# Optimization experiments

Hardware: AMD Instinct MI355X
Metric: run time of the kernel (lower is better)

## Reference

```python
import jax, jax.numpy as jnp
import numpy as np

N_NODES = 50000
N_FEAT = 128
HIDDEN = 3
N_EDGES = 600000
N_POWERS = 3


def setup_inputs() -> dict:
    key = jax.random.key(0)
    ks = jax.random.split(key, 6)
    x = jax.random.normal(ks[0], (N_NODES, N_FEAT), dtype=jnp.float32)
    edge_index = jax.random.randint(ks[1], (N_POWERS, 2, N_EDGES), 0, N_NODES, dtype=jnp.int64)
    # MLP params for the 3 adjacency powers, stacked on the leading axis.
    # torch Linear(in,out) stored transposed here: y = x @ W + b.
    Wa = jax.random.normal(ks[2], (N_POWERS, N_FEAT, HIDDEN), dtype=jnp.float32) * (1.0 / np.sqrt(N_FEAT))
    ba = jax.random.normal(ks[3], (N_POWERS, HIDDEN), dtype=jnp.float32) * 0.01
    Wb = jax.random.normal(ks[4], (N_POWERS, HIDDEN, 1), dtype=jnp.float32) * (1.0 / np.sqrt(HIDDEN))
    bb = jax.random.normal(ks[5], (N_POWERS, 1), dtype=jnp.float32) * 0.01
    return {"x": x, "edge_index": edge_index, "Wa": Wa, "ba": ba, "Wb": Wb, "bb": bb}


def reference(x, edge_index, Wa, ba, Wb, bb):
    # Gather source/target node features per edge, per adjacency power.
    x_j = x[edge_index[:, 0]]          # [P, E, F]
    x_i = x[edge_index[:, 1]]          # [P, E, F]
    abs_dif = jnp.abs(x_j - x_i)       # [P, E, F]
    # Tiny per-edge MLP: Linear -> ReLU -> Linear -> Sigmoid (separate params per power).
    h = jax.nn.relu(jnp.einsum('pef,pfh->peh', abs_dif, Wa) + ba[:, None, :])  # [P, E, H]
    w = jax.nn.sigmoid(jnp.einsum('peh,pho->peo', h, Wb) + bb[:, None, :])     # [P, E, 1]
    return w[..., 0]                   # [P, E] edge weights for each power
```

## Files before the change

kernel.cpp:

```cpp
#include <hip/hip_runtime.h>
#include <math.h>

#define N_NODES 50000
#define N_FEAT  128
#define N_EDGES 600000
#define N_POWERS 3

#define PAIRS 5
#define EDGES_PER_BLK (64 * PAIRS)

#define CAP 81920
#define NBUCK 8
#define CHUNK 2048
#define NCHUNK 293

typedef _Float16 half2v __attribute__((ext_vector_type(2)));
union HU { unsigned u; half2v h; };

__device__ __forceinline__ int bucket_of(int j) { return (int)(((unsigned)j * 41u) >> 18); }

__global__ __launch_bounds__(256) void conv_x_plain(const float* __restrict__ x,
                                                    unsigned* __restrict__ xh,
                                                    const float* __restrict__ Wa,
                                                    unsigned* __restrict__ wah) {
    const int t = blockIdx.x * 256 + threadIdx.x;
    const float4* x4 = (const float4*)x;
    float4 a = x4[(size_t)t * 2];
    float4 b = x4[(size_t)t * 2 + 1];
    HU p0, p1, p2, p3;
    p0.h = half2v{(_Float16)a.x, (_Float16)a.y};
    p1.h = half2v{(_Float16)a.z, (_Float16)a.w};
    p2.h = half2v{(_Float16)b.x, (_Float16)b.y};
    p3.h = half2v{(_Float16)b.z, (_Float16)b.w};
    ((uint4*)xh)[t] = uint4{p0.u, p1.u, p2.u, p3.u};
    if (blockIdx.x == 0 && threadIdx.x < 192) {
        const int tt = threadIdx.x;
        #pragma unroll
        for (int q = 0; q < 3; ++q) {
            int idx = tt + q * 192;
            int c  = idx % 3;
            int pk = idx / 3;
            int k  = pk % 64;
            int p  = pk / 64;
            float w0 = Wa[p * 384 + (2 * k) * 3 + c];
            float w1 = Wa[p * 384 + (2 * k + 1) * 3 + c];
            HU u; u.h = half2v{(_Float16)w0, (_Float16)w1};
            wah[idx] = u.u;
        }
    }
}

__global__ __launch_bounds__(256) void hist_kernel(const int* __restrict__ edge_index,
                                                   int* __restrict__ hist) {
    __shared__ int lh[NBUCK];
    const int p = blockIdx.y, chunk = blockIdx.x;
    if (threadIdx.x < NBUCK) lh[threadIdx.x] = 0;
    __syncthreads();
    const int* ej = edge_index + (size_t)p * 2 * N_EDGES;
    const int base = chunk * CHUNK;
    #pragma unroll
    for (int k = 0; k < 8; ++k) {
        const int e = base + k * 256 + threadIdx.x;
        if (e < N_EDGES) {
            const int j = __builtin_nontemporal_load(ej + e);
            atomicAdd(&lh[bucket_of(j)], 1);
        }
    }
    __syncthreads();
    if (threadIdx.x < NBUCK)
        hist[(p * NBUCK + threadIdx.x) * NCHUNK + chunk] = lh[threadIdx.x];
}

__global__ __launch_bounds__(64) void scan_hist(int* __restrict__ hist,
                                                int* __restrict__ cur) {
    const int pb = blockIdx.x;
    const int lane = threadIdx.x;
    int* h = hist + pb * NCHUNK;
    int carry = 0;
    for (int t = 0; t < NCHUNK; t += 64) {
        const int c = t + lane;
        int v = (c < NCHUNK) ? h[c] : 0;
        int s = v;
        #pragma unroll
        for (int d = 1; d < 64; d <<= 1) {
            int u = __shfl_up(s, d, 64);
            if (lane >= d) s += u;
        }
        if (c < NCHUNK) h[c] = carry + (s - v);
        carry += __shfl(s, 63, 64);
    }
    if (lane == 0) cur[pb] = carry;
}

__global__ __launch_bounds__(256) void scatter_pass(const int* __restrict__ edge_index,
                                                    const int* __restrict__ hist,
                                                    unsigned long long* __restrict__ su) {
    __shared__ int lc[NBUCK];
    const int p = blockIdx.y, chunk = blockIdx.x;
    if (threadIdx.x < NBUCK) lc[threadIdx.x] = 0;
    __syncthreads();
    const int* ej = edge_index + (size_t)p * 2 * N_EDGES;
    const int* ei = ej + N_EDGES;
    const int base = chunk * CHUNK;
    #pragma unroll
    for (int k = 0; k < 8; ++k) {
        const int e = base + k * 256 + threadIdx.x;
        if (e < N_EDGES) {
            const int j = __builtin_nontemporal_load(ej + e);
            const int i = __builtin_nontemporal_load(ei + e);
            const int b = bucket_of(j);
            const int pos = atomicAdd(&lc[b], 1);
            const int off = hist[(p * NBUCK + b) * NCHUNK + chunk];
            const size_t slot = (size_t)(p * NBUCK + b) * CAP + off + pos;
            su[slot] = (unsigned long long)(unsigned)(j | (i << 16))
                     | ((unsigned long long)e << 32);
        }
    }
}

template<int PAT>
__device__ __forceinline__ float swz(float v) {
    return __int_as_float(__builtin_amdgcn_ds_swizzle(__float_as_int(v), PAT));
}

__device__ __forceinline__ void dot3_8(const uint4& qa0, const uint4& qa1,
                                       const uint4& qb0, const uint4& qb1,
                                       const HU wa[8][3],
                                       float& h0, float& h1, float& h2) {
    unsigned ua[8] = {qa0.x, qa0.y, qa0.z, qa0.w, qa1.x, qa1.y, qa1.z, qa1.w};
    unsigned ub[8] = {qb0.x, qb0.y, qb0.z, qb0.w, qb1.x, qb1.y, qb1.z, qb1.w};
    h0 = 0.f; h1 = 0.f; h2 = 0.f;
    #pragma unroll
    for (int k = 0; k < 8; ++k) {
        HU a, b, d;
        a.u = ua[k]; b.u = ub[k];
        d.h = a.h - b.h;
        d.u &= 0x7fff7fffu;
        h0 = __builtin_amdgcn_fdot2(d.h, wa[k][0].h, h0, false);
        h1 = __builtin_amdgcn_fdot2(d.h, wa[k][1].h, h1, false);
        h2 = __builtin_amdgcn_fdot2(d.h, wa[k][2].h, h2, false);
    }
}

__global__ __launch_bounds__(256) void adj_kernel_sorted(
    const unsigned* __restrict__ xh,
    const unsigned long long* __restrict__ su,
    const int* __restrict__ cur,
    const unsigned* __restrict__ wah,
    const float* __restrict__ ba,
    const float* __restrict__ Wb,
    const float* __restrict__ bb,
    float* __restrict__ out)
{
    const int p    = blockIdx.y;
    const int b    = blockIdx.x & 7;
    const int k    = blockIdx.x >> 3;
    const int tid  = threadIdx.x;
    const int lane = tid & 63;
    const int wave = tid >> 6;
    const int sub  = lane & 7;
    const int grp  = lane >> 3;

    const int count = cur[p * NBUCK + b];
    const int base  = k * EDGES_PER_BLK;
    if (base >= count) return;

    HU wa[8][3];
    {
        const unsigned* wp = wah + ((size_t)p * 64 + sub * 8) * 3;
        #pragma unroll
        for (int kk = 0; kk < 8; ++kk) {
            wa[kk][0].u = wp[kk * 3 + 0];
            wa[kk][1].u = wp[kk * 3 + 1];
            wa[kk][2].u = wp[kk * 3 + 2];
        }
        #pragma unroll
        for (int kk = 0; kk < 8; ++kk) {
            asm volatile("" : "+v"(wa[kk][0].u), "+v"(wa[kk][1].u), "+v"(wa[kk][2].u));
        }
    }

    const float ba0 = ba[p * 3 + 0], ba1 = ba[p * 3 + 1], ba2 = ba[p * 3 + 2];
    const float wb0 = Wb[p * 3 + 0], wb1 = Wb[p * 3 + 1], wb2 = Wb[p * 3 + 2];
    const float bbp = bb[p];

    const unsigned long long* sup = su + (size_t)(p * NBUCK + b) * CAP;
    float* outp = out + (size_t)p * N_EDGES;

    const int eoff = wave * 8 + grp;
    const int roff = sub * 8;
    const int cm1  = count - 1;

    #pragma unroll
    for (int it = 0; it < PAIRS; ++it) {
        const int r1 = base + it * 64 + eoff;
        const int r2 = r1 + 32;
        const bool v1 = r1 < count;
        const bool v2 = r2 < count;
        const int s1 = min(r1, cm1);
        const int s2 = min(r2, cm1);

        const unsigned long long q1 = __builtin_nontemporal_load(sup + s1);
        const unsigned long long q2 = __builtin_nontemporal_load(sup + s2);
        const int j1 = (int)(q1 & 0xFFFFu);
        const int i1 = (int)((q1 >> 16) & 0xFFFFu);
        const int e1 = (int)(q1 >> 32);
        const int j2 = (int)(q2 & 0xFFFFu);
        const int i2 = (int)((q2 >> 16) & 0xFFFFu);
        const int e2 = (int)(q2 >> 32);

        const uint4* rj1 = (const uint4*)(xh + ((size_t)j1 << 6) + roff);
        const uint4* ri1 = (const uint4*)(xh + ((size_t)i1 << 6) + roff);
        const uint4* rj2 = (const uint4*)(xh + ((size_t)j2 << 6) + roff);
        const uint4* ri2 = (const uint4*)(xh + ((size_t)i2 << 6) + roff);
        uint4 a0 = rj1[0], a1 = rj1[1];
        uint4 b0 = ri1[0], b1 = ri1[1];
        uint4 c0 = rj2[0], c1 = rj2[1];
        uint4 d0 = ri2[0], d1 = ri2[1];

        float h0a, h1a, h2a, h0b, h1b, h2b;
        dot3_8(a0, a1, b0, b1, wa, h0a, h1a, h2a);
        dot3_8(c0, c1, d0, d1, wa, h0b, h1b, h2b);

        h0a += swz<0x041F>(h0a); h1a += swz<0x041F>(h1a); h2a += swz<0x041F>(h2a);
        h0b += swz<0x041F>(h0b); h1b += swz<0x041F>(h1b); h2b += swz<0x041F>(h2b);
        h0a += swz<0x081F>(h0a); h1a += swz<0x081F>(h1a); h2a += swz<0x081F>(h2a);
        h0b += swz<0x081F>(h0b); h1b += swz<0x081F>(h1b); h2b += swz<0x081F>(h2b);
        h0a += swz<0x101F>(h0a); h1a += swz<0x101F>(h1a); h2a += swz<0x101F>(h2a);
        h0b += swz<0x101F>(h0b); h1b += swz<0x101F>(h1b); h2b += swz<0x101F>(h2b);

        if (sub == 0) {
            if (v1) {
                float r0 = fmaxf(h0a + ba0, 0.f);
                float r1f = fmaxf(h1a + ba1, 0.f);
                float r2f = fmaxf(h2a + ba2, 0.f);
                float s  = fmaf(r0, wb0, fmaf(r1f, wb1, fmaf(r2f, wb2, bbp)));
                __builtin_nontemporal_store(1.f / (1.f + __expf(-s)), outp + e1);
            }
            if (v2) {
                float r0 = fmaxf(h0b + ba0, 0.f);
                float r1f = fmaxf(h1b + ba1, 0.f);
                float r2f = fmaxf(h2b + ba2, 0.f);
                float s  = fmaf(r0, wb0, fmaf(r1f, wb1, fmaf(r2f, wb2, bbp)));
                __builtin_nontemporal_store(1.f / (1.f + __expf(-s)), outp + e2);
            }
        }
    }
}

__global__ __launch_bounds__(256) void adj_kernel_f16(
    const unsigned* __restrict__ xh,
    const unsigned* __restrict__ wah,
    const int*   __restrict__ edge_index,
    const float* __restrict__ ba,
    const float* __restrict__ Wb,
    const float* __restrict__ bb,
    float* __restrict__ out)
{
    const int p    = blockIdx.y;
    const int tid  = threadIdx.x;
    const int lane = tid & 63;
    const int wave = tid >> 6;
    const int sub  = lane & 7;
    const int grp  = lane >> 3;

    HU wa[8][3];
    {
        const unsigned* wp = wah + ((size_t)p * 64 + sub * 8) * 3;
        #pragma unroll
        for (int k = 0; k < 8; ++k) {
            wa[k][0].u = wp[k * 3 + 0];
            wa[k][1].u = wp[k * 3 + 1];
            wa[k][2].u = wp[k * 3 + 2];
        }
        #pragma unroll
        for (int k = 0; k < 8; ++k) {
            asm volatile("" : "+v"(wa[k][0].u), "+v"(wa[k][1].u), "+v"(wa[k][2].u));
        }
    }

    const float ba0 = ba[p * 3 + 0], ba1 = ba[p * 3 + 1], ba2 = ba[p * 3 + 2];
    const float wb0 = Wb[p * 3 + 0], wb1 = Wb[p * 3 + 1], wb2 = Wb[p * 3 + 2];
    const float bbp = bb[p];

    const int* ej = edge_index + (size_t)p * 2 * N_EDGES;
    const int* ei = ej + N_EDGES;
    float* outp = out + (size_t)p * N_EDGES;

    const int e_blk = blockIdx.x * EDGES_PER_BLK;
    const int eoff  = wave * 8 + grp;
    const int roff  = sub * 8;

    #pragma unroll
    for (int it = 0; it < PAIRS; ++it) {
        const int e1 = e_blk + it * 64 + eoff;
        const int e2 = e1 + 32;
        const int j1 = __builtin_nontemporal_load(ej + e1);
        const int i1 = __builtin_nontemporal_load(ei + e1);
        const int j2 = __builtin_nontemporal_load(ej + e2);
        const int i2 = __builtin_nontemporal_load(ei + e2);

        const uint4* rj1 = (const uint4*)(xh + ((size_t)j1 << 6) + roff);
        const uint4* ri1 = (const uint4*)(xh + ((size_t)i1 << 6) + roff);
        const uint4* rj2 = (const uint4*)(xh + ((size_t)j2 << 6) + roff);
        const uint4* ri2 = (const uint4*)(xh + ((size_t)i2 << 6) + roff);
        uint4 a0 = rj1[0], a1 = rj1[1];
        uint4 b0 = ri1[0], b1 = ri1[1];
        uint4 c0 = rj2[0], c1 = rj2[1];
        uint4 d0 = ri2[0], d1 = ri2[1];

        float h0a, h1a, h2a, h0b, h1b, h2b;
        dot3_8(a0, a1, b0, b1, wa, h0a, h1a, h2a);
        dot3_8(c0, c1, d0, d1, wa, h0b, h1b, h2b);

        h0a += swz<0x041F>(h0a); h1a += swz<0x041F>(h1a); h2a += swz<0x041F>(h2a);
        h0b += swz<0x041F>(h0b); h1b += swz<0x041F>(h1b); h2b += swz<0x041F>(h2b);
        h0a += swz<0x081F>(h0a); h1a += swz<0x081F>(h1a); h2a += swz<0x081F>(h2a);
        h0b += swz<0x081F>(h0b); h1b += swz<0x081F>(h1b); h2b += swz<0x081F>(h2b);
        h0a += swz<0x101F>(h0a); h1a += swz<0x101F>(h1a); h2a += swz<0x101F>(h2a);
        h0b += swz<0x101F>(h0b); h1b += swz<0x101F>(h1b); h2b += swz<0x101F>(h2b);

        if (sub == 0) {
            float r0 = fmaxf(h0a + ba0, 0.f);
            float r1 = fmaxf(h1a + ba1, 0.f);
            float r2 = fmaxf(h2a + ba2, 0.f);
            float s  = fmaf(r0, wb0, fmaf(r1, wb1, fmaf(r2, wb2, bbp)));
            __builtin_nontemporal_store(1.f / (1.f + __expf(-s)), outp + e1);
            r0 = fmaxf(h0b + ba0, 0.f);
            r1 = fmaxf(h1b + ba1, 0.f);
            r2 = fmaxf(h2b + ba2, 0.f);
            s  = fmaf(r0, wb0, fmaf(r1, wb1, fmaf(r2, wb2, bbp)));
            __builtin_nontemporal_store(1.f / (1.f + __expf(-s)), outp + e2);
        }
    }
}

__global__ __launch_bounds__(256) void adj_kernel_f32(
    const float* __restrict__ x,
    const int*   __restrict__ edge_index,
    const float* __restrict__ Wa,
    const float* __restrict__ ba,
    const float* __restrict__ Wb,
    const float* __restrict__ bb,
    float* __restrict__ out)
{
    const int p    = blockIdx.y;
    const int tid  = threadIdx.x;
    const int lane = tid & 63;
    const int wave = tid >> 6;
    const int sub  = lane & 15;
    const int grp  = lane >> 4;
    const int f0 = sub * 8;

    const float* Wap = Wa + (size_t)p * N_FEAT * 3;
    float wa0[8], wa1[8], wa2[8];
    #pragma unroll
    for (int k = 0; k < 8; ++k) {
        wa0[k] = Wap[(f0 + k) * 3 + 0];
        wa1[k] = Wap[(f0 + k) * 3 + 1];
        wa2[k] = Wap[(f0 + k) * 3 + 2];
    }
    const float ba0 = ba[p * 3 + 0], ba1 = ba[p * 3 + 1], ba2 = ba[p * 3 + 2];
    const float wb0 = Wb[p * 3 + 0], wb1 = Wb[p * 3 + 1], wb2 = Wb[p * 3 + 2];
    const float bbp = bb[p];

    const int e = blockIdx.x * 16 + wave * 4 + grp;
    const int* ej = edge_index + (size_t)p * 2 * N_EDGES;
    const int* ei = ej + N_EDGES;
    const int j = ej[e];
    const int i = ei[e];

    const float4* xj = (const float4*)(x + (size_t)j * N_FEAT + f0);
    const float4* xi = (const float4*)(x + (size_t)i * N_FEAT + f0);
    float4 a0 = xj[0], a1 = xj[1];
    float4 b0 = xi[0], b1 = xi[1];

    float d[8];
    d[0] = fabsf(a0.x - b0.x); d[1] = fabsf(a0.y - b0.y);
    d[2] = fabsf(a0.z - b0.z); d[3] = fabsf(a0.w - b0.w);
    d[4] = fabsf(a1.x - b1.x); d[5] = fabsf(a1.y - b1.y);
    d[6] = fabsf(a1.z - b1.z); d[7] = fabsf(a1.w - b1.w);

    float h0 = 0.f, h1 = 0.f, h2 = 0.f;
    #pragma unroll
    for (int k = 0; k < 8; ++k) {
        h0 = fmaf(d[k], wa0[k], h0);
        h1 = fmaf(d[k], wa1[k], h1);
        h2 = fmaf(d[k], wa2[k], h2);
    }
    #pragma unroll
    for (int m = 1; m < 16; m <<= 1) {
        h0 += __shfl_xor(h0, m, 64);
        h1 += __shfl_xor(h1, m, 64);
        h2 += __shfl_xor(h2, m, 64);
    }
    if (sub == 0) {
        float r0 = fmaxf(h0 + ba0, 0.f);
        float r1 = fmaxf(h1 + ba1, 0.f);
        float r2 = fmaxf(h2 + ba2, 0.f);
        float s  = fmaf(r0, wb0, fmaf(r1, wb1, fmaf(r2, wb2, bbp)));
        float w  = 1.f / (1.f + expf(-s));
        out[(size_t)p * N_EDGES + e] = w;
    }
}

extern "C" void kernel_launch(void* const* d_in, const int* in_sizes, int n_in,
                              void* d_out, int out_size, void* d_ws, size_t ws_size,
                              hipStream_t stream) {
    const float* x          = (const float*)d_in[0];
    const int*   edge_index = (const int*)d_in[1];
    const float* Wa         = (const float*)d_in[2];
    const float* ba         = (const float*)d_in[3];
    const float* Wb         = (const float*)d_in[4];
    const float* bb         = (const float*)d_in[5];
    float* out = (float*)d_out;

    const size_t x_bytes    = (size_t)N_NODES * N_FEAT * 2;
    const size_t su_bytes   = (size_t)N_POWERS * NBUCK * CAP * 8;
    const size_t wa_bytes   = 2304;
    const size_t hist_bytes = (size_t)N_POWERS * NBUCK * NCHUNK * 4;
    const size_t cur_bytes  = NBUCK * N_POWERS * 4;
    const size_t need_full  = x_bytes + su_bytes + wa_bytes + hist_bytes + cur_bytes;

    if (ws_size >= need_full) {
        char* w = (char*)d_ws;
        unsigned* xh = (unsigned*)w;
        unsigned long long* su = (unsigned long long*)(w + x_bytes);
        unsigned* wah = (unsigned*)(w + x_bytes + su_bytes);
        int* hist = (int*)(w + x_bytes + su_bytes + wa_bytes);
        int* cur  = (int*)(w + x_bytes + su_bytes + wa_bytes + hist_bytes);

        conv_x_plain<<<N_NODES * N_FEAT / 2048, 256, 0, stream>>>(x, xh, Wa, wah);
        hist_kernel<<<dim3(NCHUNK, N_POWERS), 256, 0, stream>>>(edge_index, hist);
        scan_hist<<<NBUCK * N_POWERS, 64, 0, stream>>>(hist, cur);
        scatter_pass<<<dim3(NCHUNK, N_POWERS), 256, 0, stream>>>(edge_index, hist, su);
        dim3 grid(NBUCK * (CAP / EDGES_PER_BLK), N_POWERS);
        adj_kernel_sorted<<<grid, 256, 0, stream>>>(xh, su, cur, wah, ba, Wb, bb, out);
    } else if (ws_size >= x_bytes + wa_bytes) {
        unsigned* xh  = (unsigned*)d_ws;
        unsigned* wah = (unsigned*)((char*)d_ws + x_bytes);
        conv_x_plain<<<N_NODES * N_FEAT / 2048, 256, 0, stream>>>(x, xh, Wa, wah);
        dim3 grid(N_EDGES / EDGES_PER_BLK, N_POWERS);
        adj_kernel_f16<<<grid, 256, 0, stream>>>(xh, wah, edge_index, ba, Wb, bb, out);
    } else {
        dim3 grid((N_EDGES + 15) / 16, N_POWERS);
        adj_kernel_f32<<<grid, 256, 0, stream>>>(x, edge_index, Wa, ba, Wb, bb, out);
    }
}
```

Measured before the change: 177.3 us.

## Aggregate bucket atomics per wave and software-pipeline gathers in sorted adjacency kernel

The histogram and scatter passes now group lanes by bucket using ballots. One leader per bucket does a single LDS atomic for the whole group, and scatter computes each lane's rank with popcount. The scatter pass also seeds its local counters with the chunk offsets, so it no longer reads hist per edge. The sorted adjacency kernel preloads all packed edge records up front and prefetches the next iteration's node feature rows while computing the current one, under a launch-bounds occupancy hint. This aims to cut LDS atomic contention and hide gather latency, at the cost of extra registers.

```diff
diff --git a/kernel.cpp b/kernel.cpp
--- a/kernel.cpp
+++ b/kernel.cpp
@@ -18,6 +18,17 @@
 union HU { unsigned u; half2v h; };
 
 __device__ __forceinline__ int bucket_of(int j) { return (int)(((unsigned)j * 41u) >> 18); }
+
+__device__ __forceinline__ unsigned long long match8(int b, bool valid) {
+    const unsigned long long m0 = __ballot(b & 1);
+    const unsigned long long m1 = __ballot(b & 2);
+    const unsigned long long m2 = __ballot(b & 4);
+    const unsigned long long vm = __ballot(valid);
+    unsigned long long m = (b & 1) ? m0 : ~m0;
+    m &= (b & 2) ? m1 : ~m1;
+    m &= (b & 4) ? m2 : ~m2;
+    return m & vm;
+}
 
 __global__ __launch_bounds__(256) void conv_x_plain(const float* __restrict__ x,
                                                     unsigned* __restrict__ xh,
@@ -58,13 +69,16 @@
     __syncthreads();
     const int* ej = edge_index + (size_t)p * 2 * N_EDGES;
     const int base = chunk * CHUNK;
+    const int lane = threadIdx.x & 63;
     #pragma unroll
     for (int k = 0; k < 8; ++k) {
         const int e = base + k * 256 + threadIdx.x;
-        if (e < N_EDGES) {
-            const int j = __builtin_nontemporal_load(ej + e);
-            atomicAdd(&lh[bucket_of(j)], 1);
-        }
+        const bool valid = e < N_EDGES;
+        const int j = __builtin_nontemporal_load(ej + (valid ? e : 0));
+        const int b = bucket_of(j);
+        const unsigned long long m = match8(b, valid);
+        if (valid && lane == (int)__builtin_ctzll(m))
+            atomicAdd(&lh[b], (int)__popcll(m));
     }
     __syncthreads();
     if (threadIdx.x < NBUCK)
@@ -97,21 +111,29 @@
                                                     unsigned long long* __restrict__ su) {
     __shared__ int lc[NBUCK];
     const int p = blockIdx.y, chunk = blockIdx.x;
-    if (threadIdx.x < NBUCK) lc[threadIdx.x] = 0;
+    if (threadIdx.x < NBUCK)
+        lc[threadIdx.x] = hist[(p * NBUCK + threadIdx.x) * NCHUNK + chunk];
     __syncthreads();
     const int* ej = edge_index + (size_t)p * 2 * N_EDGES;
     const int* ei = ej + N_EDGES;
     const int base = chunk * CHUNK;
+    const int lane = threadIdx.x & 63;
     #pragma unroll
     for (int k = 0; k < 8; ++k) {
         const int e = base + k * 256 + threadIdx.x;
-        if (e < N_EDGES) {
-            const int j = __builtin_nontemporal_load(ej + e);
-            const int i = __builtin_nontemporal_load(ei + e);
-            const int b = bucket_of(j);
-            const int pos = atomicAdd(&lc[b], 1);
-            const int off = hist[(p * NBUCK + b) * NCHUNK + chunk];
-            const size_t slot = (size_t)(p * NBUCK + b) * CAP + off + pos;
+        const bool valid = e < N_EDGES;
+        const int j = __builtin_nontemporal_load(ej + (valid ? e : 0));
+        const int i = __builtin_nontemporal_load(ei + (valid ? e : 0));
+        const int b = bucket_of(j);
+        const unsigned long long m = match8(b, valid);
+        const int ldr = m ? (int)__builtin_ctzll(m) : 0;
+        int basepos = 0;
+        if (valid && lane == ldr)
+            basepos = atomicAdd(&lc[b], (int)__popcll(m));
+        basepos = __shfl(basepos, ldr, 64);
+        if (valid) {
+            const int rank = (int)__popcll(m & ((1ull << lane) - 1ull));
+            const size_t slot = (size_t)(p * NBUCK + b) * CAP + basepos + rank;
             su[slot] = (unsigned long long)(unsigned)(j | (i << 16))
                      | ((unsigned long long)e << 32);
         }
@@ -142,7 +164,7 @@
     }
 }
 
-__global__ __launch_bounds__(256) void adj_kernel_sorted(
+__global__ __launch_bounds__(256, 4) void adj_kernel_sorted(
     const unsigned* __restrict__ xh,
     const unsigned long long* __restrict__ su,
     const int* __restrict__ cur,
@@ -191,36 +213,43 @@
     const int roff = sub * 8;
     const int cm1  = count - 1;
 
+    unsigned long long q[2 * PAIRS];
     #pragma unroll
     for (int it = 0; it < PAIRS; ++it) {
         const int r1 = base + it * 64 + eoff;
-        const int r2 = r1 + 32;
-        const bool v1 = r1 < count;
-        const bool v2 = r2 < count;
-        const int s1 = min(r1, cm1);
-        const int s2 = min(r2, cm1);
-
-        const unsigned long long q1 = __builtin_nontemporal_load(sup + s1);
-        const unsigned long long q2 = __builtin_nontemporal_load(sup + s2);
-        const int j1 = (int)(q1 & 0xFFFFu);
-        const int i1 = (int)((q1 >> 16) & 0xFFFFu);
-        const int e1 = (int)(q1 >> 32);
-        const int j2 = (int)(q2 & 0xFFFFu);
-        const int i2 = (int)((q2 >> 16) & 0xFFFFu);
-        const int e2 = (int)(q2 >> 32);
-
+        q[2 * it]     = __builtin_nontemporal_load(sup + min(r1, cm1));
+        q[2 * it + 1] = __builtin_nontemporal_load(sup + min(r1 + 32, cm1));
+    }
+
+    uint4 A0, A1, B0, B1, C0, C1, D0, D1;
+    {
+        const int j1 = (int)(q[0] & 0xFFFFu), i1 = (int)((q[0] >> 16) & 0xFFFFu);
+        const int j2 = (int)(q[1] & 0xFFFFu), i2 = (int)((q[1] >> 16) & 0xFFFFu);
         const uint4* rj1 = (const uint4*)(xh + ((size_t)j1 << 6) + roff);
         const uint4* ri1 = (const uint4*)(xh + ((size_t)i1 << 6) + roff);
         const uint4* rj2 = (const uint4*)(xh + ((size_t)j2 << 6) + roff);
         const uint4* ri2 = (const uint4*)(xh + ((size_t)i2 << 6) + roff);
-        uint4 a0 = rj1[0], a1 = rj1[1];
-        uint4 b0 = ri1[0], b1 = ri1[1];
-        uint4 c0 = rj2[0], c1 = rj2[1];
-        uint4 d0 = ri2[0], d1 = ri2[1];
+        A0 = rj1[0]; A1 = rj1[1]; B0 = ri1[0]; B1 = ri1[1];
+        C0 = rj2[0]; C1 = rj2[1]; D0 = ri2[0]; D1 = ri2[1];
+    }
+
+    #pragma unroll
+    for (int it = 0; it < PAIRS; ++it) {
+        uint4 nA0, nA1, nB0, nB1, nC0, nC1, nD0, nD1;
+        if (it + 1 < PAIRS) {
+            const int j1 = (int)(q[2 * it + 2] & 0xFFFFu), i1 = (int)((q[2 * it + 2] >> 16) & 0xFFFFu);
+            const int j2 = (int)(q[2 * it + 3] & 0xFFFFu), i2 = (int)((q[2 * it + 3] >> 16) & 0xFFFFu);
+            const uint4* rj1 = (const uint4*)(xh + ((size_t)j1 << 6) + roff);
+            const uint4* ri1 = (const uint4*)(xh + ((size_t)i1 << 6) + roff);
+            const uint4* rj2 = (const uint4*)(xh + ((size_t)j2 << 6) + roff);
+            const uint4* ri2 = (const uint4*)(xh + ((size_t)i2 << 6) + roff);
+            nA0 = rj1[0]; nA1 = rj1[1]; nB0 = ri1[0]; nB1 = ri1[1];
+            nC0 = rj2[0]; nC1 = rj2[1]; nD0 = ri2[0]; nD1 = ri2[1];
+        }
 
         float h0a, h1a, h2a, h0b, h1b, h2b;
-        dot3_8(a0, a1, b0, b1, wa, h0a, h1a, h2a);
-        dot3_8(c0, c1, d0, d1, wa, h0b, h1b, h2b);
+        dot3_8(A0, A1, B0, B1, wa, h0a, h1a, h2a);
+        dot3_8(C0, C1, D0, D1, wa, h0b, h1b, h2b);
 
         h0a += swz<0x041F>(h0a); h1a += swz<0x041F>(h1a); h2a += swz<0x041F>(h2a);
         h0b += swz<0x041F>(h0b); h1b += swz<0x041F>(h1b); h2b += swz<0x041F>(h2b);
@@ -230,20 +259,29 @@
         h0b += swz<0x101F>(h0b); h1b += swz<0x101F>(h1b); h2b += swz<0x101F>(h2b);
 
         if (sub == 0) {
-            if (v1) {
-                float r0 = fmaxf(h0a + ba0, 0.f);
+            const int r1 = base + it * 64 + eoff;
+            const int r2 = r1 + 32;
+            if (r1 < count) {
+                const int e1 = (int)(q[2 * it] >> 32);
+                float r0  = fmaxf(h0a + ba0, 0.f);
                 float r1f = fmaxf(h1a + ba1, 0.f);
                 float r2f = fmaxf(h2a + ba2, 0.f);
-                float s  = fmaf(r0, wb0, fmaf(r1f, wb1, fmaf(r2f, wb2, bbp)));
+                float s   = fmaf(r0, wb0, fmaf(r1f, wb1, fmaf(r2f, wb2, bbp)));
                 __builtin_nontemporal_store(1.f / (1.f + __expf(-s)), outp + e1);
             }
-            if (v2) {
-                float r0 = fmaxf(h0b + ba0, 0.f);
+            if (r2 < count) {
+                const int e2 = (int)(q[2 * it + 1] >> 32);
+                float r0  = fmaxf(h0b + ba0, 0.f);
                 float r1f = fmaxf(h1b + ba1, 0.f);
                 float r2f = fmaxf(h2b + ba2, 0.f);
-                float s  = fmaf(r0, wb0, fmaf(r1f, wb1, fmaf(r2f, wb2, bbp)));
+                float s   = fmaf(r0, wb0, fmaf(r1f, wb1, fmaf(r2f, wb2, bbp)));
                 __builtin_nontemporal_store(1.f / (1.f + __expf(-s)), outp + e2);
             }
+        }
+
+        if (it + 1 < PAIRS) {
+            A0 = nA0; A1 = nA1; B0 = nB0; B1 = nB1;
+            C0 = nC0; C1 = nC1; D0 = nD0; D1 = nD1;
         }
     }
 }
```

Result: no change. 175.0 us (-1.3%).

## Replace bucket sort with full counting sort by source node and unscatter outputs

Applied to the files above, without the earlier changes.

Swaps the 8-bucket partial sort for a full counting sort of edges by source node: per-node atomic counts, a 50k-element block scan, and an atomic scatter that also records each edge's inverse slot. The main kernel then walks edges in fully sorted order so the source-row gathers reuse cache, and it software-pipelines the next pair of row loads. Results are written in sorted order over the key buffer and permuted back by a new unscatter kernel. The cost is two extra launches, global atomics on node counters, a single-block-per-power serial scan, and a random-read gather pass for the outputs.

```diff
diff --git a/kernel.cpp b/kernel.cpp
--- a/kernel.cpp
+++ b/kernel.cpp
@@ -9,20 +9,15 @@
 #define PAIRS 5
 #define EDGES_PER_BLK (64 * PAIRS)
 
-#define CAP 81920
-#define NBUCK 8
-#define CHUNK 2048
-#define NCHUNK 293
-
 typedef _Float16 half2v __attribute__((ext_vector_type(2)));
+typedef unsigned u32x4  __attribute__((ext_vector_type(4)));
 union HU { unsigned u; half2v h; };
-
-__device__ __forceinline__ int bucket_of(int j) { return (int)(((unsigned)j * 41u) >> 18); }
 
 __global__ __launch_bounds__(256) void conv_x_plain(const float* __restrict__ x,
                                                     unsigned* __restrict__ xh,
                                                     const float* __restrict__ Wa,
-                                                    unsigned* __restrict__ wah) {
+                                                    unsigned* __restrict__ wah,
+                                                    int* __restrict__ cnt) {
     const int t = blockIdx.x * 256 + threadIdx.x;
     const float4* x4 = (const float4*)x;
     float4 a = x4[(size_t)t * 2];
@@ -33,6 +28,8 @@
     p2.h = half2v{(_Float16)b.x, (_Float16)b.y};
     p3.h = half2v{(_Float16)b.z, (_Float16)b.w};
     ((uint4*)xh)[t] = uint4{p0.u, p1.u, p2.u, p3.u};
+    if (cnt != nullptr && t < N_POWERS * N_NODES)
+        cnt[t] = 0;
     if (blockIdx.x == 0 && threadIdx.x < 192) {
         const int tt = threadIdx.x;
         #pragma unroll
@@ -50,72 +47,62 @@
     }
 }
 
-__global__ __launch_bounds__(256) void hist_kernel(const int* __restrict__ edge_index,
-                                                   int* __restrict__ hist) {
-    __shared__ int lh[NBUCK];
-    const int p = blockIdx.y, chunk = blockIdx.x;
-    if (threadIdx.x < NBUCK) lh[threadIdx.x] = 0;
+__global__ __launch_bounds__(1024) void count_kernel(const int* __restrict__ edge_index,
+                                                     int* __restrict__ cnt) {
+    const int p = blockIdx.y;
+    const int e = blockIdx.x * 1024 + threadIdx.x;
+    if (e >= N_EDGES) return;
+    const int j = __builtin_nontemporal_load(edge_index + (size_t)p * 2 * N_EDGES + e);
+    atomicAdd(cnt + p * N_NODES + j, 1);
+}
+
+__global__ __launch_bounds__(1024) void scan50k(int* __restrict__ cnt) {
+    const int p = blockIdx.x;
+    int* c = cnt + p * N_NODES;
+    const int tid = threadIdx.x;
+    const int t0 = tid * 49;
+    const int n  = (t0 >= N_NODES) ? 0 : ((N_NODES - t0 < 49) ? (N_NODES - t0) : 49);
+
+    int s = 0;
+    for (int k = 0; k < n; ++k) s += c[t0 + k];
+
+    const int lane = tid & 63, wv = tid >> 6;
+    int ps = s;
+    #pragma unroll
+    for (int d = 1; d < 64; d <<= 1) {
+        int u = __shfl_up(ps, d, 64);
+        if (lane >= d) ps += u;
+    }
+    __shared__ int wsum[16];
+    if (lane == 63) wsum[wv] = ps;
     __syncthreads();
+    if (tid == 0) {
+        int acc = 0;
+        #pragma unroll
+        for (int w = 0; w < 16; ++w) { int t = wsum[w]; wsum[w] = acc; acc += t; }
+    }
+    __syncthreads();
+    int run = wsum[wv] + (ps - s);
+    for (int k = 0; k < n; ++k) {
+        int t = c[t0 + k];
+        c[t0 + k] = run;
+        run += t;
+    }
+}
+
+__global__ __launch_bounds__(1024) void scatter_sort(const int* __restrict__ edge_index,
+                                                     int* __restrict__ cnt,
+                                                     unsigned* __restrict__ su,
+                                                     int* __restrict__ inv) {
+    const int p = blockIdx.y;
+    const int e = blockIdx.x * 1024 + threadIdx.x;
+    if (e >= N_EDGES) return;
     const int* ej = edge_index + (size_t)p * 2 * N_EDGES;
-    const int base = chunk * CHUNK;
-    #pragma unroll
-    for (int k = 0; k < 8; ++k) {
-        const int e = base + k * 256 + threadIdx.x;
-        if (e < N_EDGES) {
-            const int j = __builtin_nontemporal_load(ej + e);
-            atomicAdd(&lh[bucket_of(j)], 1);
-        }
-    }
-    __syncthreads();
-    if (threadIdx.x < NBUCK)
-        hist[(p * NBUCK + threadIdx.x) * NCHUNK + chunk] = lh[threadIdx.x];
-}
-
-__global__ __launch_bounds__(64) void scan_hist(int* __restrict__ hist,
-                                                int* __restrict__ cur) {
-    const int pb = blockIdx.x;
-    const int lane = threadIdx.x;
-    int* h = hist + pb * NCHUNK;
-    int carry = 0;
-    for (int t = 0; t < NCHUNK; t += 64) {
-        const int c = t + lane;
-        int v = (c < NCHUNK) ? h[c] : 0;
-        int s = v;
-        #pragma unroll
-        for (int d = 1; d < 64; d <<= 1) {
-            int u = __shfl_up(s, d, 64);
-            if (lane >= d) s += u;
-        }
-        if (c < NCHUNK) h[c] = carry + (s - v);
-        carry += __shfl(s, 63, 64);
-    }
-    if (lane == 0) cur[pb] = carry;
-}
-
-__global__ __launch_bounds__(256) void scatter_pass(const int* __restrict__ edge_index,
-                                                    const int* __restrict__ hist,
-                                                    unsigned long long* __restrict__ su) {
-    __shared__ int lc[NBUCK];
-    const int p = blockIdx.y, chunk = blockIdx.x;
-    if (threadIdx.x < NBUCK) lc[threadIdx.x] = 0;
-    __syncthreads();
-    const int* ej = edge_index + (size_t)p * 2 * N_EDGES;
-    const int* ei = ej + N_EDGES;
-    const int base = chunk * CHUNK;
-    #pragma unroll
-    for (int k = 0; k < 8; ++k) {
-        const int e = base + k * 256 + threadIdx.x;
-        if (e < N_EDGES) {
-            const int j = __builtin_nontemporal_load(ej + e);
-            const int i = __builtin_nontemporal_load(ei + e);
-            const int b = bucket_of(j);
-            const int pos = atomicAdd(&lc[b], 1);
-            const int off = hist[(p * NBUCK + b) * NCHUNK + chunk];
-            const size_t slot = (size_t)(p * NBUCK + b) * CAP + off + pos;
-            su[slot] = (unsigned long long)(unsigned)(j | (i << 16))
-                     | ((unsigned long long)e << 32);
-        }
-    }
+    const int j = __builtin_nontemporal_load(ej + e);
+    const int i = __builtin_nontemporal_load(ej + N_EDGES + e);
+    const int slot = atomicAdd(cnt + p * N_NODES + j, 1);
+    su[(size_t)p * N_EDGES + slot] = (unsigned)j | ((unsigned)i << 16);
+    inv[(size_t)p * N_EDGES + e] = slot;
 }
 
 template<int PAT>
@@ -123,12 +110,12 @@
     return __int_as_float(__builtin_amdgcn_ds_swizzle(__float_as_int(v), PAT));
 }
 
-__device__ __forceinline__ void dot3_8(const uint4& qa0, const uint4& qa1,
-                                       const uint4& qb0, const uint4& qb1,
+__device__ __forceinline__ void dot3_8(const u32x4& qa0, const u32x4& qa1,
+                                       const u32x4& qb0, const u32x4& qb1,
                                        const HU wa[8][3],
                                        float& h0, float& h1, float& h2) {
-    unsigned ua[8] = {qa0.x, qa0.y, qa0.z, qa0.w, qa1.x, qa1.y, qa1.z, qa1.w};
-    unsigned ub[8] = {qb0.x, qb0.y, qb0.z, qb0.w, qb1.x, qb1.y, qb1.z, qb1.w};
+    unsigned ua[8] = {qa0[0], qa0[1], qa0[2], qa0[3], qa1[0], qa1[1], qa1[2], qa1[3]};
+    unsigned ub[8] = {qb0[0], qb0[1], qb0[2], qb0[3], qb1[0], qb1[1], qb1[2], qb1[3]};
     h0 = 0.f; h1 = 0.f; h2 = 0.f;
     #pragma unroll
     for (int k = 0; k < 8; ++k) {
@@ -142,28 +129,22 @@
     }
 }
 
-__global__ __launch_bounds__(256) void adj_kernel_sorted(
+__global__ __launch_bounds__(256, 4) void adj_kernel_sorted(
     const unsigned* __restrict__ xh,
-    const unsigned long long* __restrict__ su,
-    const int* __restrict__ cur,
+    unsigned* su,
     const unsigned* __restrict__ wah,
     const float* __restrict__ ba,
     const float* __restrict__ Wb,
-    const float* __restrict__ bb,
-    float* __restrict__ out)
+    const float* __restrict__ bb)
 {
     const int p    = blockIdx.y;
-    const int b    = blockIdx.x & 7;
-    const int k    = blockIdx.x >> 3;
     const int tid  = threadIdx.x;
     const int lane = tid & 63;
     const int wave = tid >> 6;
     const int sub  = lane & 7;
     const int grp  = lane >> 3;
 
-    const int count = cur[p * NBUCK + b];
-    const int base  = k * EDGES_PER_BLK;
-    if (base >= count) return;
+    const int base = blockIdx.x * EDGES_PER_BLK;
 
     HU wa[8][3];
     {
@@ -184,43 +165,52 @@
     const float wb0 = Wb[p * 3 + 0], wb1 = Wb[p * 3 + 1], wb2 = Wb[p * 3 + 2];
     const float bbp = bb[p];
 
-    const unsigned long long* sup = su + (size_t)(p * NBUCK + b) * CAP;
-    float* outp = out + (size_t)p * N_EDGES;
+    unsigned* sup = su + (size_t)p * N_EDGES;
 
     const int eoff = wave * 8 + grp;
     const int roff = sub * 8;
-    const int cm1  = count - 1;
-
+
+    unsigned q[2 * PAIRS];
     #pragma unroll
     for (int it = 0; it < PAIRS; ++it) {
         const int r1 = base + it * 64 + eoff;
-        const int r2 = r1 + 32;
-        const bool v1 = r1 < count;
-        const bool v2 = r2 < count;
-        const int s1 = min(r1, cm1);
-        const int s2 = min(r2, cm1);
-
-        const unsigned long long q1 = __builtin_nontemporal_load(sup + s1);
-        const unsigned long long q2 = __builtin_nontemporal_load(sup + s2);
-        const int j1 = (int)(q1 & 0xFFFFu);
-        const int i1 = (int)((q1 >> 16) & 0xFFFFu);
-        const int e1 = (int)(q1 >> 32);
-        const int j2 = (int)(q2 & 0xFFFFu);
-        const int i2 = (int)((q2 >> 16) & 0xFFFFu);
-        const int e2 = (int)(q2 >> 32);
-
-        const uint4* rj1 = (const uint4*)(xh + ((size_t)j1 << 6) + roff);
-        const uint4* ri1 = (const uint4*)(xh + ((size_t)i1 << 6) + roff);
-        const uint4* rj2 = (const uint4*)(xh + ((size_t)j2 << 6) + roff);
-        const uint4* ri2 = (const uint4*)(xh + ((size_t)i2 << 6) + roff);
-        uint4 a0 = rj1[0], a1 = rj1[1];
-        uint4 b0 = ri1[0], b1 = ri1[1];
-        uint4 c0 = rj2[0], c1 = rj2[1];
-        uint4 d0 = ri2[0], d1 = ri2[1];
+        q[2 * it]     = __builtin_nontemporal_load(sup + r1);
+        q[2 * it + 1] = __builtin_nontemporal_load(sup + r1 + 32);
+    }
+
+    u32x4 A0, A1, B0, B1, C0, C1, D0, D1;
+    {
+        const int j1 = (int)(q[0] & 0xFFFFu), i1 = (int)(q[0] >> 16);
+        const int j2 = (int)(q[1] & 0xFFFFu), i2 = (int)(q[1] >> 16);
+        const u32x4* rj1 = (const u32x4*)(xh + ((size_t)j1 << 6) + roff);
+        const u32x4* ri1 = (const u32x4*)(xh + ((size_t)i1 << 6) + roff);
+        const u32x4* rj2 = (const u32x4*)(xh + ((size_t)j2 << 6) + roff);
+        const u32x4* ri2 = (const u32x4*)(xh + ((size_t)i2 << 6) + roff);
+        A0 = rj1[0]; A1 = rj1[1];
+        B0 = __builtin_nontemporal_load(ri1); B1 = __builtin_nontemporal_load(ri1 + 1);
+        C0 = rj2[0]; C1 = rj2[1];
+        D0 = __builtin_nontemporal_load(ri2); D1 = __builtin_nontemporal_load(ri2 + 1);
+    }
+
+    #pragma unroll
+    for (int it = 0; it < PAIRS; ++it) {
+        u32x4 nA0, nA1, nB0, nB1, nC0, nC1, nD0, nD1;
+        if (it + 1 < PAIRS) {
+            const int j1 = (int)(q[2 * it + 2] & 0xFFFFu), i1 = (int)(q[2 * it + 2] >> 16);
+            const int j2 = (int)(q[2 * it + 3] & 0xFFFFu), i2 = (int)(q[2 * it + 3] >> 16);
+            const u32x4* rj1 = (const u32x4*)(xh + ((size_t)j1 << 6) + roff);
+            const u32x4* ri1 = (const u32x4*)(xh + ((size_t)i1 << 6) + roff);
+            const u32x4* rj2 = (const u32x4*)(xh + ((size_t)j2 << 6) + roff);
+            const u32x4* ri2 = (const u32x4*)(xh + ((size_t)i2 << 6) + roff);
+            nA0 = rj1[0]; nA1 = rj1[1];
+            nB0 = __builtin_nontemporal_load(ri1); nB1 = __builtin_nontemporal_load(ri1 + 1);
+            nC0 = rj2[0]; nC1 = rj2[1];
+            nD0 = __builtin_nontemporal_load(ri2); nD1 = __builtin_nontemporal_load(ri2 + 1);
+        }
 
         float h0a, h1a, h2a, h0b, h1b, h2b;
-        dot3_8(a0, a1, b0, b1, wa, h0a, h1a, h2a);
-        dot3_8(c0, c1, d0, d1, wa, h0b, h1b, h2b);
+        dot3_8(A0, A1, B0, B1, wa, h0a, h1a, h2a);
+        dot3_8(C0, C1, D0, D1, wa, h0b, h1b, h2b);
 
         h0a += swz<0x041F>(h0a); h1a += swz<0x041F>(h1a); h2a += swz<0x041F>(h2a);
         h0b += swz<0x041F>(h0b); h1b += swz<0x041F>(h1b); h2b += swz<0x041F>(h2b);
@@ -230,22 +220,41 @@
         h0b += swz<0x101F>(h0b); h1b += swz<0x101F>(h1b); h2b += swz<0x101F>(h2b);
 
         if (sub == 0) {
-            if (v1) {
-                float r0 = fmaxf(h0a + ba0, 0.f);
+            const int r1 = base + it * 64 + eoff;
+            {
+                float r0  = fmaxf(h0a + ba0, 0.f);
                 float r1f = fmaxf(h1a + ba1, 0.f);
                 float r2f = fmaxf(h2a + ba2, 0.f);
-                float s  = fmaf(r0, wb0, fmaf(r1f, wb1, fmaf(r2f, wb2, bbp)));
-                __builtin_nontemporal_store(1.f / (1.f + __expf(-s)), outp + e1);
+                float s   = fmaf(r0, wb0, fmaf(r1f, wb1, fmaf(r2f, wb2, bbp)));
+                __builtin_nontemporal_store(1.f / (1.f + __expf(-s)), (float*)sup + r1);
             }
-            if (v2) {
-                float r0 = fmaxf(h0b + ba0, 0.f);
+            {
+                float r0  = fmaxf(h0b + ba0, 0.f);
                 float r1f = fmaxf(h1b + ba1, 0.f);
                 float r2f = fmaxf(h2b + ba2, 0.f);
-                float s  = fmaf(r0, wb0, fmaf(r1f, wb1, fmaf(r2f, wb2, bbp)));
-                __builtin_nontemporal_store(1.f / (1.f + __expf(-s)), outp + e2);
+                float s   = fmaf(r0, wb0, fmaf(r1f, wb1, fmaf(r2f, wb2, bbp)));
+                __builtin_nontemporal_store(1.f / (1.f + __expf(-s)), (float*)sup + r1 + 32);
             }
         }
-    }
+
+        if (it + 1 < PAIRS) {
+            A0 = nA0; A1 = nA1; B0 = nB0; B1 = nB1;
+            C0 = nC0; C1 = nC1; D0 = nD0; D1 = nD1;
+        }
+    }
+}
+
+__global__ __launch_bounds__(256) void unscatter_kernel(const unsigned* __restrict__ su,
+                                                        const int* __restrict__ inv,
+                                                        float* __restrict__ out) {
+    const int p  = blockIdx.y;
+    const int t4 = (blockIdx.x * 256 + threadIdx.x) * 4;
+    if (t4 >= N_EDGES) return;
+    const int4 iv = *(const int4*)(inv + (size_t)p * N_EDGES + t4);
+    const float* w = (const float*)(su + (size_t)p * N_EDGES);
+    float4 o;
+    o.x = w[iv.x]; o.y = w[iv.y]; o.z = w[iv.z]; o.w = w[iv.w];
+    *(float4*)(out + (size_t)p * N_EDGES + t4) = o;
 }
 
 __global__ __launch_bounds__(256) void adj_kernel_f16(
@@ -300,14 +309,14 @@
         const int j2 = __builtin_nontemporal_load(ej + e2);
         const int i2 = __builtin_nontemporal_load(ei + e2);
 
-        const uint4* rj1 = (const uint4*)(xh + ((size_t)j1 << 6) + roff);
-        const uint4* ri1 = (const uint4*)(xh + ((size_t)i1 << 6) + roff);
-        const uint4* rj2 = (const uint4*)(xh + ((size_t)j2 << 6) + roff);
-        const uint4* ri2 = (const uint4*)(xh + ((size_t)i2 << 6) + roff);
-        uint4 a0 = rj1[0], a1 = rj1[1];
-        uint4 b0 = ri1[0], b1 = ri1[1];
-        uint4 c0 = rj2[0], c1 = rj2[1];
-        uint4 d0 = ri2[0], d1 = ri2[1];
+        const u32x4* rj1 = (const u32x4*)(xh + ((size_t)j1 << 6) + roff);
+        const u32x4* ri1 = (const u32x4*)(xh + ((size_t)i1 << 6) + roff);
+        const u32x4* rj2 = (const u32x4*)(xh + ((size_t)j2 << 6) + roff);
+        const u32x4* ri2 = (const u32x4*)(xh + ((size_t)i2 << 6) + roff);
+        u32x4 a0 = rj1[0], a1 = rj1[1];
+        u32x4 b0 = ri1[0], b1 = ri1[1];
+        u32x4 c0 = rj2[0], c1 = rj2[1];
+        u32x4 d0 = ri2[0], d1 = ri2[1];
 
         float h0a, h1a, h2a, h0b, h1b, h2b;
         dot3_8(a0, a1, b0, b1, wa, h0a, h1a, h2a);
@@ -415,31 +424,34 @@
     const float* bb         = (const float*)d_in[5];
     float* out = (float*)d_out;
 
-    const size_t x_bytes    = (size_t)N_NODES * N_FEAT * 2;
-    const size_t su_bytes   = (size_t)N_POWERS * NBUCK * CAP * 8;
-    const size_t wa_bytes   = 2304;
-    const size_t hist_bytes = (size_t)N_POWERS * NBUCK * NCHUNK * 4;
-    const size_t cur_bytes  = NBUCK * N_POWERS * 4;
-    const size_t need_full  = x_bytes + su_bytes + wa_bytes + hist_bytes + cur_bytes;
+    const size_t x_bytes   = (size_t)N_NODES * N_FEAT * 2;
+    const size_t su_bytes  = (size_t)N_POWERS * N_EDGES * 4;
+    const size_t inv_bytes = (size_t)N_POWERS * N_EDGES * 4;
+    const size_t wa_bytes  = 2304;
+    const size_t cnt_bytes = (size_t)N_POWERS * N_NODES * 4;
+    const size_t need_full = x_bytes + su_bytes + inv_bytes + wa_bytes + cnt_bytes;
 
     if (ws_size >= need_full) {
         char* w = (char*)d_ws;
-        unsigned* xh = (unsigned*)w;
-        unsigned long long* su = (unsigned long long*)(w + x_bytes);
-        unsigned* wah = (unsigned*)(w + x_bytes + su_bytes);
-        int* hist = (int*)(w + x_bytes + su_bytes + wa_bytes);
-        int* cur  = (int*)(w + x_bytes + su_bytes + wa_bytes + hist_bytes);
-
-        conv_x_plain<<<N_NODES * N_FEAT / 2048, 256, 0, stream>>>(x, xh, Wa, wah);
-        hist_kernel<<<dim3(NCHUNK, N_POWERS), 256, 0, stream>>>(edge_index, hist);
-        scan_hist<<<NBUCK * N_POWERS, 64, 0, stream>>>(hist, cur);
-        scatter_pass<<<dim3(NCHUNK, N_POWERS), 256, 0, stream>>>(edge_index, hist, su);
-        dim3 grid(NBUCK * (CAP / EDGES_PER_BLK), N_POWERS);
-        adj_kernel_sorted<<<grid, 256, 0, stream>>>(xh, su, cur, wah, ba, Wb, bb, out);
+        unsigned* xh  = (unsigned*)w;
+        unsigned* su  = (unsigned*)(w + x_bytes);
+        int*      inv = (int*)(w + x_bytes + su_bytes);
+        unsigned* wah = (unsigned*)(w + x_bytes + su_bytes + inv_bytes);
+        int*      cnt = (int*)(w + x_bytes + su_bytes + inv_bytes + wa_bytes);
+
+        const int egrid = (N_EDGES + 1023) / 1024;
+        conv_x_plain<<<N_NODES * N_FEAT / 2048, 256, 0, stream>>>(x, xh, Wa, wah, cnt);
+        count_kernel<<<dim3(egrid, N_POWERS), 1024, 0, stream>>>(edge_index, cnt);
+        scan50k<<<N_POWERS, 1024, 0, stream>>>(cnt);
+        scatter_sort<<<dim3(egrid, N_POWERS), 1024, 0, stream>>>(edge_index, cnt, su, inv);
+        adj_kernel_sorted<<<dim3(N_EDGES / EDGES_PER_BLK, N_POWERS), 256, 0, stream>>>(
+            xh, su, wah, ba, Wb, bb);
+        unscatter_kernel<<<dim3((N_EDGES / 4 + 255) / 256, N_POWERS), 256, 0, stream>>>(
+            su, inv, out);
     } else if (ws_size >= x_bytes + wa_bytes) {
         unsigned* xh  = (unsigned*)d_ws;
         unsigned* wah = (unsigned*)((char*)d_ws + x_bytes);
-        conv_x_plain<<<N_NODES * N_FEAT / 2048, 256, 0, stream>>>(x, xh, Wa, wah);
+        conv_x_plain<<<N_NODES * N_FEAT / 2048, 256, 0, stream>>>(x, xh, Wa, wah, nullptr);
         dim3 grid(N_EDGES / EDGES_PER_BLK, N_POWERS);
         adj_kernel_f16<<<grid, 256, 0, stream>>>(xh, wah, edge_index, ba, Wb, bb, out);
     } else {
```

Result: slower. 474.1 us (+167.4%).
